# Kernel tuning notes

Measured on AMD Instinct MI355X. Metric: run time of the kernel, lower is better.

The kernel has to match this reference:

```python
import jax, jax.numpy as jnp
import numpy as np

N = 100000          # nodes
E = 1600000         # edges (avg degree 16)
F_IN = 128          # input node features
H1, C1 = 8, 8       # conv1: 8 heads, 8 channels/head -> 64 concat
NUM_CLASSES = 40    # conv2: 1 head, 40 channels
EPS = 1e-16         # PyG softmax denominator epsilon
NEG_SLOPE = 0.2     # PyG GATConv default leaky_relu slope


def setup_inputs() -> dict:
    key = jax.random.key(0)
    ks = jax.random.split(key, 12)
    x = jax.random.normal(ks[0], (N, F_IN), jnp.float32)
    edge_index = jax.random.randint(ks[1], (2, E), 0, N, dtype=jnp.int64)
    edge_attr = jax.random.normal(ks[2], (E, 1), jnp.float32)
    # layer 1 params (Glorot-ish scaling)
    s1 = 1.0 / np.sqrt(F_IN)
    W1 = jax.random.normal(ks[3], (F_IN, H1 * C1), jnp.float32) * s1
    a_src1 = jax.random.normal(ks[4], (H1, C1), jnp.float32) * (1.0 / np.sqrt(C1))
    a_dst1 = jax.random.normal(ks[5], (H1, C1), jnp.float32) * (1.0 / np.sqrt(C1))
    b1 = jnp.zeros((H1 * C1,), jnp.float32)
    # layer 2 params: in = 64 (conv1 concat output), 1 head, NUM_CLASSES channels
    s2 = 1.0 / np.sqrt(H1 * C1)
    W2 = jax.random.normal(ks[6], (H1 * C1, NUM_CLASSES), jnp.float32) * s2
    a_src2 = jax.random.normal(ks[7], (1, NUM_CLASSES), jnp.float32) * (1.0 / np.sqrt(NUM_CLASSES))
    a_dst2 = jax.random.normal(ks[8], (1, NUM_CLASSES), jnp.float32) * (1.0 / np.sqrt(NUM_CLASSES))
    b2 = jnp.zeros((NUM_CLASSES,), jnp.float32)
    return {"x": x, "edge_index": edge_index, "edge_attr": edge_attr,
            "W1": W1, "a_src1": a_src1, "a_dst1": a_dst1, "b1": b1,
            "W2": W2, "a_src2": a_src2, "a_dst2": a_dst2, "b2": b2}


def gat_conv(x, src, dst, W, a_s, a_d, b, heads, out_ch):
    """PyG GATConv: linear -> per-edge leaky-relu attention -> dst softmax -> scatter-add."""
    n = x.shape[0]
    h = (x @ W).reshape(n, heads, out_ch)                 # [N,H,C]
    alpha_s = jnp.sum(h * a_s, axis=-1)                   # [N,H]
    alpha_d = jnp.sum(h * a_d, axis=-1)                   # [N,H]
    e = jax.nn.leaky_relu(alpha_s[src] + alpha_d[dst], NEG_SLOPE)  # [Etot,H]
    # segment softmax over incoming edges per destination node
    m = jax.ops.segment_max(e, dst, num_segments=n)       # [N,H]
    e = jnp.exp(e - m[dst])
    denom = jax.ops.segment_sum(e, dst, num_segments=n)   # [N,H]
    alpha = e / (denom[dst] + EPS)                        # [Etot,H]
    msg = h[src] * alpha[:, :, None]                      # [Etot,H,C]
    out = jax.ops.segment_sum(msg, dst, num_segments=n)   # [N,H,C]
    return out.reshape(n, heads * out_ch) + b             # concat heads + bias


def reference(x, edge_index, edge_attr, W1, a_src1, a_dst1, b1, W2, a_src2, a_dst2, b2):
    n = x.shape[0]
    # PyG GATConv adds self-loops by default
    loops = jnp.arange(n, dtype=edge_index.dtype)
    src = jnp.concatenate([edge_index[0], loops])
    dst = jnp.concatenate([edge_index[1], loops])
    x = x.astype(jnp.float32)
    x1 = jax.nn.elu(gat_conv(x, src, dst, W1, a_src1, a_dst1, b1, H1, C1))
    x2 = jax.nn.elu(gat_conv(x1, src, dst, W2, a_src2, a_dst2, b2, 1, NUM_CLASSES))
    return x2
```

## Files before the change

### kernel.cpp

```cpp
#include <hip/hip_runtime.h>
#include <math.h>

#define NN 100000
#define NE 1600000
#define NETOT (NE + NN)
#define FIN 128
#define H1N 8
#define D1 64
#define NC 40
#define LNT 64
#define LOG2E 1.44269504088896f

#define BSH 9
#define BNODES 512
#define NBUC ((NN + BNODES - 1) / BNODES)
#define EPB 4096
#define NBLKA ((NE + EPB - 1) / EPB)
#define BCAP 9216
#define LB1 ((NN + LNT - 1) / LNT)

__device__ __forceinline__ float leakyf(float x) { return x >= 0.0f ? x : 0.2f * x; }
__device__ __forceinline__ float eluf(float x)   { return x > 0.0f ? x : expm1f(x); }
__device__ __forceinline__ float exp2fast(float x) { return __builtin_amdgcn_exp2f(x); }

__device__ __forceinline__ unsigned short f2bf(float f) {
  unsigned u = __float_as_uint(f);
  u += 0x7fffu + ((u >> 16) & 1u);
  return (unsigned short)(u >> 16);
}
__device__ __forceinline__ float bflo(unsigned u) { return __uint_as_float(u << 16); }
__device__ __forceinline__ float bfhi(unsigned u) { return __uint_as_float(u & 0xffff0000u); }

__global__ void k_detect(const long long* __restrict__ ei, int* __restrict__ flag) {
  if (blockIdx.x == 0 && threadIdx.x == 0) {
    int is64 = 1;
    for (int i = 0; i < 16; ++i) {
      long long v = ei[i];
      if (v < 0 || v >= NN) is64 = 0;
    }
    *flag = is64;
  }
}

#define XS1(node, k) xs[(node) * FIN + ((k) ^ ((node) & 31))]
__global__ __launch_bounds__(512) void k_fusedA(
    const void* __restrict__ ei, const int* __restrict__ flag,
    unsigned int* __restrict__ subbuf, int* __restrict__ bcnt,
    const float* __restrict__ x, const float* __restrict__ W,
    const float* __restrict__ aw_s, const float* __restrict__ aw_d,
    unsigned short* __restrict__ h, float* __restrict__ als,
    float* __restrict__ ald) {
  __shared__ __align__(16) char smem[65536];
  int t = threadIdx.x;
  if (blockIdx.x < NBLKA) {
    unsigned int*   pay    = (unsigned int*)smem;
    unsigned int*   spay   = pay + EPB;
    unsigned short* bk     = (unsigned short*)(spay + EPB);
    unsigned short* sbk    = bk + EPB;
    int*            hist   = (int*)(sbk + EPB);
    int*            lstart = hist + 256;
    int*            cur    = lstart + 256;
    int*            gbase  = cur + 256;
    int e0 = blockIdx.x * EPB;
    int cnt = min(EPB, NE - e0);
    if (t < 256) hist[t] = 0;
    __syncthreads();
    bool f64 = (*flag) != 0;
    for (int i = t; i < cnt; i += 512) {
      int s, d;
      if (f64) {
        const long long* p = (const long long*)ei;
        s = (int)p[e0 + i]; d = (int)p[NE + e0 + i];
      } else {
        const int* p = (const int*)ei;
        s = p[e0 + i]; d = p[NE + e0 + i];
      }
      int b = d >> BSH;
      pay[i] = ((unsigned)s << BSH) | (unsigned)(d & (BNODES - 1));
      bk[i] = (unsigned short)b;
      atomicAdd(&hist[b], 1);
    }
    __syncthreads();
    int v = 0;
    if (t < 256) { v = hist[t]; lstart[t] = v; }
    __syncthreads();
    for (int st = 1; st < 256; st <<= 1) {
      int xv = (t < 256 && t >= st) ? lstart[t - st] : 0;
      __syncthreads();
      if (t < 256) lstart[t] += xv;
      __syncthreads();
    }
    int excl = 0;
    if (t < 256) excl = lstart[t] - v;
    __syncthreads();
    if (t < 256) {
      lstart[t] = excl;
      cur[t] = excl;
      gbase[t] = (v > 0) ? atomicAdd(&bcnt[t], v) : 0;
    }
    __syncthreads();
    for (int i = t; i < cnt; i += 512) {
      int b = bk[i];
      int pos = atomicAdd(&cur[b], 1);
      spay[pos] = pay[i];
      sbk[pos] = (unsigned short)b;
    }
    __syncthreads();
    for (int i = t; i < cnt; i += 512) {
      int b = sbk[i];
      int o = gbase[b] + (i - lstart[b]);
      if (o < BCAP) subbuf[(size_t)b * BCAP + o] = spay[i];
    }
  } else {
    float* ws = (float*)smem;
    float* xs = ws + FIN * D1;
    int base = (blockIdx.x - NBLKA) * LNT;
    for (int i = t; i < FIN * D1; i += 512) ws[i] = W[i];
    for (int i = t; i < LNT * FIN; i += 512) {
      int node = i >> 7, k = i & 127;
      int gn = base + node;
      if (gn >= NN) gn = NN - 1;
      XS1(node, k) = x[(size_t)gn * FIN + k];
    }
    __syncthreads();
    int head = t & 7, nl = t >> 3;
    float acc[8] = {0, 0, 0, 0, 0, 0, 0, 0};
    #pragma unroll 4
    for (int k = 0; k < FIN; ++k) {
      float x0 = XS1(nl, k);
      const float4* wr = (const float4*)&ws[k * D1 + head * 8];
      float4 wa = wr[0], wb = wr[1];
      acc[0] = fmaf(x0, wa.x, acc[0]);
      acc[1] = fmaf(x0, wa.y, acc[1]);
      acc[2] = fmaf(x0, wa.z, acc[2]);
      acc[3] = fmaf(x0, wa.w, acc[3]);
      acc[4] = fmaf(x0, wb.x, acc[4]);
      acc[5] = fmaf(x0, wb.y, acc[5]);
      acc[6] = fmaf(x0, wb.z, acc[6]);
      acc[7] = fmaf(x0, wb.w, acc[7]);
    }
    int n0 = base + nl;
    if (n0 < NN) {
      float s = 0.f, d = 0.f;
      #pragma unroll
      for (int c = 0; c < 8; ++c) {
        h[(size_t)n0 * D1 + head * 8 + c] = f2bf(acc[c]);
        s = fmaf(acc[c], aw_s[head * 8 + c], s);
        d = fmaf(acc[c], aw_d[head * 8 + c], d);
      }
      als[n0 * H1N + head] = s * LOG2E;
      ald[n0 * H1N + head] = d * LOG2E;
    }
  }
}

__global__ void k_bucketsum(const int* __restrict__ bcnt, int* __restrict__ bucket_base,
                            int* __restrict__ row_start) {
  __shared__ int sh[256];
  int t = threadIdx.x;
  int tot = 0;
  if (t < NBUC) {
    int d0 = t << BSH;
    int nloc = min(BNODES, NN - d0);
    tot = nloc + min(bcnt[t], BCAP);
  }
  sh[t] = tot;
  __syncthreads();
  for (int s = 1; s < 256; s <<= 1) {
    int x = (t >= s) ? sh[t - s] : 0;
    __syncthreads();
    sh[t] += x;
    __syncthreads();
  }
  if (t < NBUC) bucket_base[t] = sh[t] - tot;
  if (t == NBUC - 1) row_start[NN] = sh[t];
}

__global__ __launch_bounds__(256) void k_passB(const int* __restrict__ bcnt,
                       const unsigned int* __restrict__ subbuf,
                       const int* __restrict__ bucket_base,
                       int* __restrict__ row_start, int* __restrict__ csr) {
  __shared__ int hist[BNODES];
  __shared__ int ps[256];
  __shared__ int cur[BNODES];
  int b = blockIdx.x, t = threadIdx.x;
  int d0 = b << BSH;
  int nloc = min(BNODES, NN - d0);
  hist[t] = 0; hist[t + 256] = 0;
  __syncthreads();
  int cnt = min(bcnt[b], BCAP);
  const unsigned int* sb = subbuf + (size_t)b * BCAP;
  for (int i = t; i < cnt; i += 256)
    atomicAdd(&hist[sb[i] & (BNODES - 1)], 1);
  __syncthreads();
  int j0 = 2 * t, j1 = 2 * t + 1;
  int s0 = (j0 < nloc) ? hist[j0] + 1 : 0;
  int s1 = (j1 < nloc) ? hist[j1] + 1 : 0;
  int pairsum = s0 + s1;
  ps[t] = pairsum;
  __syncthreads();
  for (int s = 1; s < 256; s <<= 1) {
    int x = (t >= s) ? ps[t - s] : 0;
    __syncthreads();
    ps[t] += x;
    __syncthreads();
  }
  int excl = ps[t] - pairsum + bucket_base[b];
  if (j0 < nloc) {
    row_start[d0 + j0] = excl;
    csr[excl] = d0 + j0;
    cur[j0] = excl + 1;
  }
  if (j1 < nloc) {
    int rs = excl + s0;
    row_start[d0 + j1] = rs;
    csr[rs] = d0 + j1;
    cur[j1] = rs + 1;
  }
  __syncthreads();
  for (int i = t; i < cnt; i += 256) {
    unsigned u = sb[i];
    int pos = atomicAdd(&cur[u & (BNODES - 1)], 1);
    csr[pos] = (int)(u >> BSH);
  }
}

#define XS2(node, k) xs[(node) * D1 + ((k) ^ ((node) & 31))]
__global__ __launch_bounds__(512) void k_lin2(
    const unsigned int* __restrict__ x1bf, const float* __restrict__ W,
    const float* __restrict__ aw_s, const float* __restrict__ aw_d,
    unsigned short* __restrict__ h, float* __restrict__ als,
    float* __restrict__ ald) {
  __shared__ float ws[D1 * D1];
  __shared__ float xs[LNT * D1];
  int t = threadIdx.x;
  int base = blockIdx.x * LNT;
  for (int i = t; i < D1 * D1; i += 512) {
    int k = i >> 6, c = i & 63;
    ws[i] = (c < NC) ? W[k * NC + c] : 0.f;
  }
  for (int i = t; i < LNT * 32; i += 512) {
    int node = i >> 5, kd = i & 31;
    int gn = base + node;
    if (gn >= NN) gn = NN - 1;
    unsigned u = x1bf[(size_t)gn * 32 + kd];
    XS2(node, 2 * kd)     = bflo(u);
    XS2(node, 2 * kd + 1) = bfhi(u);
  }
  __syncthreads();
  int g = t & 7, nl = t >> 3;
  float acc[8] = {0, 0, 0, 0, 0, 0, 0, 0};
  #pragma unroll 4
  for (int k = 0; k < D1; ++k) {
    float x0 = XS2(nl, k);
    const float4* wr = (const float4*)&ws[k * D1 + g * 8];
    float4 wa = wr[0], wb = wr[1];
    acc[0] = fmaf(x0, wa.x, acc[0]);
    acc[1] = fmaf(x0, wa.y, acc[1]);
    acc[2] = fmaf(x0, wa.z, acc[2]);
    acc[3] = fmaf(x0, wa.w, acc[3]);
    acc[4] = fmaf(x0, wb.x, acc[4]);
    acc[5] = fmaf(x0, wb.y, acc[5]);
    acc[6] = fmaf(x0, wb.z, acc[6]);
    acc[7] = fmaf(x0, wb.w, acc[7]);
  }
  int n0 = base + nl;
  float s = 0.f, d = 0.f;
  #pragma unroll
  for (int c = 0; c < 8; ++c) {
    int col = g * 8 + c;
    float aws = (col < NC) ? aw_s[col] : 0.f;
    float awd = (col < NC) ? aw_d[col] : 0.f;
    s = fmaf(acc[c], aws, s);
    d = fmaf(acc[c], awd, d);
  }
  s += __shfl_xor(s, 1); d += __shfl_xor(d, 1);
  s += __shfl_xor(s, 2); d += __shfl_xor(d, 2);
  s += __shfl_xor(s, 4); d += __shfl_xor(d, 4);
  if (n0 < NN) {
    if (g < 5) {
      #pragma unroll
      for (int c = 0; c < 8; ++c) h[(size_t)n0 * NC + g * 8 + c] = f2bf(acc[c]);
    }
    if (g == 0) { als[n0] = s * LOG2E; ald[n0] = d * LOG2E; }
  }
}

__global__ void k_node1(const int* __restrict__ row_start, const int* __restrict__ csr,
                        const unsigned short* __restrict__ h, const float* __restrict__ als,
                        const float* __restrict__ ald, const float* __restrict__ b,
                        unsigned int* __restrict__ x1bf) {
  __shared__ float pl[4][2][32 * 9];
  int wid = threadIdx.x >> 6, half = (threadIdx.x >> 5) & 1, c2 = threadIdx.x & 31;
  int n = blockIdx.x * 8 + wid * 2 + half;
  float* pw = pl[wid][half];
  const unsigned int* h32 = (const unsigned int*)h;
  int r0 = row_start[n], r1 = row_start[n + 1];
  int hd = c2 >> 2;
  const float4* adp = (const float4*)(ald + (size_t)n * H1N);
  float4 ad0 = adp[0], ad1 = adp[1];
  float S = 0.f;
  float alo0 = 0.f, ahi0 = 0.f, alo1 = 0.f, ahi1 = 0.f;
  float alo2 = 0.f, ahi2 = 0.f, alo3 = 0.f, ahi3 = 0.f;
  for (int kb = r0; kb < r1; kb += 32) {
    int cnt = min(32, r1 - kb);
    if (c2 < cnt) {
      int sk = csr[kb + c2];
      const float4* ap = (const float4*)(als + (size_t)sk * H1N);
      float4 a0 = ap[0], a1 = ap[1];
      pw[c2 * 9 + 0] = exp2fast(leakyf(a0.x + ad0.x));
      pw[c2 * 9 + 1] = exp2fast(leakyf(a0.y + ad0.y));
      pw[c2 * 9 + 2] = exp2fast(leakyf(a0.z + ad0.z));
      pw[c2 * 9 + 3] = exp2fast(leakyf(a0.w + ad0.w));
      pw[c2 * 9 + 4] = exp2fast(leakyf(a1.x + ad1.x));
      pw[c2 * 9 + 5] = exp2fast(leakyf(a1.y + ad1.y));
      pw[c2 * 9 + 6] = exp2fast(leakyf(a1.z + ad1.z));
      pw[c2 * 9 + 7] = exp2fast(leakyf(a1.w + ad1.w));
      pw[c2 * 9 + 8] = __int_as_float(sk);
    }
    asm volatile("s_waitcnt lgkmcnt(0)" ::: "memory");
    int j = 0;
    for (; j + 4 <= cnt; j += 4) {
      int s0 = __float_as_int(pw[(j + 0) * 9 + 8]);
      int s1 = __float_as_int(pw[(j + 1) * 9 + 8]);
      int s2 = __float_as_int(pw[(j + 2) * 9 + 8]);
      int s3 = __float_as_int(pw[(j + 3) * 9 + 8]);
      float p0 = pw[(j + 0) * 9 + hd], p1 = pw[(j + 1) * 9 + hd];
      float p2 = pw[(j + 2) * 9 + hd], p3 = pw[(j + 3) * 9 + hd];
      unsigned u0 = h32[(unsigned)s0 * 32 + c2];
      unsigned u1 = h32[(unsigned)s1 * 32 + c2];
      unsigned u2 = h32[(unsigned)s2 * 32 + c2];
      unsigned u3 = h32[(unsigned)s3 * 32 + c2];
      alo0 = fmaf(p0, bflo(u0), alo0); ahi0 = fmaf(p0, bfhi(u0), ahi0);
      alo1 = fmaf(p1, bflo(u1), alo1); ahi1 = fmaf(p1, bfhi(u1), ahi1);
      alo2 = fmaf(p2, bflo(u2), alo2); ahi2 = fmaf(p2, bfhi(u2), ahi2);
      alo3 = fmaf(p3, bflo(u3), alo3); ahi3 = fmaf(p3, bfhi(u3), ahi3);
      S += (p0 + p1) + (p2 + p3);
    }
    for (; j < cnt; ++j) {
      int s0 = __float_as_int(pw[j * 9 + 8]);
      float p0 = pw[j * 9 + hd];
      unsigned u0 = h32[(unsigned)s0 * 32 + c2];
      alo0 = fmaf(p0, bflo(u0), alo0); ahi0 = fmaf(p0, bfhi(u0), ahi0);
      S += p0;
    }
  }
  float alo = (alo0 + alo1) + (alo2 + alo3);
  float ahi = (ahi0 + ahi1) + (ahi2 + ahi3);
  float inv = 1.0f / (S + 1e-16f);
  float ox = eluf(alo * inv + b[2 * c2 + 0]);
  float oy = eluf(ahi * inv + b[2 * c2 + 1]);
  x1bf[(size_t)n * 32 + c2] = (unsigned)f2bf(ox) | ((unsigned)f2bf(oy) << 16);
}

__global__ void k_node2(const int* __restrict__ row_start, const int* __restrict__ csr,
                        const unsigned short* __restrict__ h, const float* __restrict__ als,
                        const float* __restrict__ ald, const float* __restrict__ b,
                        float* __restrict__ out) {
  __shared__ float pl[4][2][32 * 3];
  int wid = threadIdx.x >> 6, half = (threadIdx.x >> 5) & 1, c2 = threadIdx.x & 31;
  int n = blockIdx.x * 8 + wid * 2 + half;
  float* pw = pl[wid][half];
  const unsigned int* h32 = (const unsigned int*)h;
  int r0 = row_start[n], r1 = row_start[n + 1];
  int cl = c2 < 20 ? c2 : 19;
  float aldn = ald[n];
  float S = 0.f;
  float alo0 = 0.f, ahi0 = 0.f, alo1 = 0.f, ahi1 = 0.f;
  float alo2 = 0.f, ahi2 = 0.f, alo3 = 0.f, ahi3 = 0.f;
  for (int kb = r0; kb < r1; kb += 32) {
    int cnt = min(32, r1 - kb);
    if (c2 < cnt) {
      int sk = csr[kb + c2];
      pw[c2 * 3 + 0] = exp2fast(leakyf(als[sk] + aldn));
      pw[c2 * 3 + 1] = __int_as_float(sk);
    }
    asm volatile("s_waitcnt lgkmcnt(0)" ::: "memory");
    int j = 0;
    for (; j + 4 <= cnt; j += 4) {
      int s0 = __float_as_int(pw[(j + 0) * 3 + 1]);
      int s1 = __float_as_int(pw[(j + 1) * 3 + 1]);
      int s2 = __float_as_int(pw[(j + 2) * 3 + 1]);
      int s3 = __float_as_int(pw[(j + 3) * 3 + 1]);
      float p0 = pw[(j + 0) * 3], p1 = pw[(j + 1) * 3];
      float p2 = pw[(j + 2) * 3], p3 = pw[(j + 3) * 3];
      unsigned u0 = h32[(unsigned)s0 * 20 + cl];
      unsigned u1 = h32[(unsigned)s1 * 20 + cl];
      unsigned u2 = h32[(unsigned)s2 * 20 + cl];
      unsigned u3 = h32[(unsigned)s3 * 20 + cl];
      alo0 = fmaf(p0, bflo(u0), alo0); ahi0 = fmaf(p0, bfhi(u0), ahi0);
      alo1 = fmaf(p1, bflo(u1), alo1); ahi1 = fmaf(p1, bfhi(u1), ahi1);
      alo2 = fmaf(p2, bflo(u2), alo2); ahi2 = fmaf(p2, bfhi(u2), ahi2);
      alo3 = fmaf(p3, bflo(u3), alo3); ahi3 = fmaf(p3, bfhi(u3), ahi3);
      S += (p0 + p1) + (p2 + p3);
    }
    for (; j < cnt; ++j) {
      int s0 = __float_as_int(pw[j * 3 + 1]);
      float p0 = pw[j * 3];
      unsigned u0 = h32[(unsigned)s0 * 20 + cl];
      alo0 = fmaf(p0, bflo(u0), alo0); ahi0 = fmaf(p0, bfhi(u0), ahi0);
      S += p0;
    }
  }
  float alo = (alo0 + alo1) + (alo2 + alo3);
  float ahi = (ahi0 + ahi1) + (ahi2 + ahi3);
  if (c2 < 20) {
    float inv = 1.0f / (S + 1e-16f);
    float2 o;
    o.x = eluf(alo * inv + b[2 * c2 + 0]);
    o.y = eluf(ahi * inv + b[2 * c2 + 1]);
    ((float2*)out)[(size_t)n * 20 + c2] = o;
  }
}

extern "C" void kernel_launch(void* const* d_in, const int* in_sizes, int n_in,
                              void* d_out, int out_size, void* d_ws, size_t ws_size,
                              hipStream_t stream) {
  const float* x    = (const float*)d_in[0];
  const void*  ei   = d_in[1];
  const float* W1   = (const float*)d_in[3];
  const float* as1w = (const float*)d_in[4];
  const float* ad1w = (const float*)d_in[5];
  const float* b1   = (const float*)d_in[6];
  const float* W2   = (const float*)d_in[7];
  const float* as2w = (const float*)d_in[8];
  const float* ad2w = (const float*)d_in[9];
  const float* b2   = (const float*)d_in[10];
  float* out = (float*)d_out;

  char* w = (char*)d_ws;
  size_t off = 0;
  auto carve = [&](size_t bytes) -> void* {
    void* r = w + off;
    off += (bytes + 255) & ~(size_t)255;
    return r;
  };
  int*            flag        = (int*)carve(256);
  int*            bcnt        = (int*)carve((size_t)NBUC * 4);
  int*            bucket_base = (int*)carve((size_t)NBUC * 4);
  unsigned int*   subbuf      = (unsigned int*)carve((size_t)NBUC * BCAP * 4);
  int*            row_start   = (int*)carve((size_t)(NN + 1) * 4);
  int*            csr         = (int*)carve((size_t)NETOT * 4);
  unsigned short* h1          = (unsigned short*)carve((size_t)NN * D1 * 2);
  float*          als1        = (float*)carve((size_t)NN * H1N * 4);
  float*          ald1        = (float*)carve((size_t)NN * H1N * 4);
  unsigned int*   x1bf        = (unsigned int*)carve((size_t)NN * 32 * 4);
  unsigned short* h2 = h1; float* als2 = als1; float* ald2 = ald1;

  k_detect<<<1, 64, 0, stream>>>((const long long*)ei, flag);
  (void)hipMemsetAsync(bcnt, 0, (size_t)NBUC * 4, stream);

  k_fusedA<<<NBLKA + LB1, 512, 0, stream>>>(ei, flag, subbuf, bcnt,
                                            x, W1, as1w, ad1w, h1, als1, ald1);

  k_bucketsum<<<1, 256, 0, stream>>>(bcnt, bucket_base, row_start);
  k_passB<<<NBUC, 256, 0, stream>>>(bcnt, subbuf, bucket_base, row_start, csr);

  k_node1<<<NN / 8, 256, 0, stream>>>(row_start, csr, h1, als1, ald1, b1, x1bf);

  k_lin2<<<LB1, 512, 0, stream>>>(x1bf, W2, as2w, ad2w, h2, als2, ald2);
  k_node2<<<NN / 8, 256, 0, stream>>>(row_start, csr, h2, als2, ald2, b2, out);
}
```

Measured before the change: 206.2 us.

## Fold memset and bucket scan into neighbor kernels, repack node2 lanes, vectorize h store

Zeroing the bucket counters moves into the detect kernel, and the separate bucket-sum kernel is removed: every passB block redoes the small prefix scan over bucket totals itself. This cuts two launches or dependent steps. k_node2 now packs three destination nodes per wavefront, 20 lanes each, instead of two nodes per 32 lanes with 12 idle lanes, which raises lane use in the 40-class aggregation. The layer-1 bf16 h write becomes one 16-byte packed store per thread instead of eight 2-byte stores. In exchange, each passB block repeats the scan redundantly, and 4 of 64 lanes stay idle in node2.

```diff
diff --git a/kernel.cpp b/kernel.cpp
--- a/kernel.cpp
+++ b/kernel.cpp
@@ -17,7 +17,7 @@
 #define EPB 4096
 #define NBLKA ((NE + EPB - 1) / EPB)
 #define BCAP 9216
-#define LB1 ((NN + LNT - 1) / LNT)
+#define LB ((NN + LNT - 1) / LNT)
 
 __device__ __forceinline__ float leakyf(float x) { return x >= 0.0f ? x : 0.2f * x; }
 __device__ __forceinline__ float eluf(float x)   { return x > 0.0f ? x : expm1f(x); }
@@ -31,8 +31,11 @@
 __device__ __forceinline__ float bflo(unsigned u) { return __uint_as_float(u << 16); }
 __device__ __forceinline__ float bfhi(unsigned u) { return __uint_as_float(u & 0xffff0000u); }
 
-__global__ void k_detect(const long long* __restrict__ ei, int* __restrict__ flag) {
-  if (blockIdx.x == 0 && threadIdx.x == 0) {
+__global__ void k_detect(const long long* __restrict__ ei, int* __restrict__ flag,
+                         int* __restrict__ bcnt) {
+  int t = threadIdx.x;
+  if (t < NBUC) bcnt[t] = 0;
+  if (t == 0) {
     int is64 = 1;
     for (int i = 0; i < 16; ++i) {
       long long v = ei[i];
@@ -123,12 +126,12 @@
       XS1(node, k) = x[(size_t)gn * FIN + k];
     }
     __syncthreads();
-    int head = t & 7, nl = t >> 3;
+    int g = t & 7, nl = t >> 3;
     float acc[8] = {0, 0, 0, 0, 0, 0, 0, 0};
     #pragma unroll 4
     for (int k = 0; k < FIN; ++k) {
       float x0 = XS1(nl, k);
-      const float4* wr = (const float4*)&ws[k * D1 + head * 8];
+      const float4* wr = (const float4*)&ws[k * D1 + g * 8];
       float4 wa = wr[0], wb = wr[1];
       acc[0] = fmaf(x0, wa.x, acc[0]);
       acc[1] = fmaf(x0, wa.y, acc[1]);
@@ -142,50 +145,50 @@
     int n0 = base + nl;
     if (n0 < NN) {
       float s = 0.f, d = 0.f;
+      uint4 pk;
+      pk.x = (unsigned)f2bf(acc[0]) | ((unsigned)f2bf(acc[1]) << 16);
+      pk.y = (unsigned)f2bf(acc[2]) | ((unsigned)f2bf(acc[3]) << 16);
+      pk.z = (unsigned)f2bf(acc[4]) | ((unsigned)f2bf(acc[5]) << 16);
+      pk.w = (unsigned)f2bf(acc[6]) | ((unsigned)f2bf(acc[7]) << 16);
+      *(uint4*)(void*)(h + (size_t)n0 * D1 + g * 8) = pk;
       #pragma unroll
       for (int c = 0; c < 8; ++c) {
-        h[(size_t)n0 * D1 + head * 8 + c] = f2bf(acc[c]);
-        s = fmaf(acc[c], aw_s[head * 8 + c], s);
-        d = fmaf(acc[c], aw_d[head * 8 + c], d);
+        s = fmaf(acc[c], aw_s[g * 8 + c], s);
+        d = fmaf(acc[c], aw_d[g * 8 + c], d);
       }
-      als[n0 * H1N + head] = s * LOG2E;
-      ald[n0 * H1N + head] = d * LOG2E;
-    }
-  }
-}
-
-__global__ void k_bucketsum(const int* __restrict__ bcnt, int* __restrict__ bucket_base,
-                            int* __restrict__ row_start) {
-  __shared__ int sh[256];
-  int t = threadIdx.x;
-  int tot = 0;
-  if (t < NBUC) {
-    int d0 = t << BSH;
-    int nloc = min(BNODES, NN - d0);
-    tot = nloc + min(bcnt[t], BCAP);
-  }
-  sh[t] = tot;
-  __syncthreads();
-  for (int s = 1; s < 256; s <<= 1) {
-    int x = (t >= s) ? sh[t - s] : 0;
-    __syncthreads();
-    sh[t] += x;
-    __syncthreads();
-  }
-  if (t < NBUC) bucket_base[t] = sh[t] - tot;
-  if (t == NBUC - 1) row_start[NN] = sh[t];
+      als[n0 * H1N + g] = s * LOG2E;
+      ald[n0 * H1N + g] = d * LOG2E;
+    }
+  }
 }
 
 __global__ __launch_bounds__(256) void k_passB(const int* __restrict__ bcnt,
                        const unsigned int* __restrict__ subbuf,
-                       const int* __restrict__ bucket_base,
                        int* __restrict__ row_start, int* __restrict__ csr) {
   __shared__ int hist[BNODES];
   __shared__ int ps[256];
   __shared__ int cur[BNODES];
+  __shared__ int bbs;
   int b = blockIdx.x, t = threadIdx.x;
   int d0 = b << BSH;
   int nloc = min(BNODES, NN - d0);
+  int tot = 0;
+  if (t < NBUC) {
+    int dd = t << BSH;
+    tot = min(BNODES, NN - dd) + min(bcnt[t], BCAP);
+  }
+  ps[t] = tot;
+  __syncthreads();
+  for (int s = 1; s < 256; s <<= 1) {
+    int xv = (t >= s) ? ps[t - s] : 0;
+    __syncthreads();
+    ps[t] += xv;
+    __syncthreads();
+  }
+  if (t == 0) bbs = (b == 0) ? 0 : ps[b - 1];
+  if (b == 0 && t == 0) row_start[NN] = ps[NBUC - 1];
+  __syncthreads();
+  int bucket_base = bbs;
   hist[t] = 0; hist[t + 256] = 0;
   __syncthreads();
   int cnt = min(bcnt[b], BCAP);
@@ -205,7 +208,7 @@
     ps[t] += x;
     __syncthreads();
   }
-  int excl = ps[t] - pairsum + bucket_base[b];
+  int excl = ps[t] - pairsum + bucket_base;
   if (j0 < nloc) {
     row_start[d0 + j0] = excl;
     csr[excl] = d0 + j0;
@@ -357,37 +360,40 @@
                         const unsigned short* __restrict__ h, const float* __restrict__ als,
                         const float* __restrict__ ald, const float* __restrict__ b,
                         float* __restrict__ out) {
-  __shared__ float pl[4][2][32 * 3];
-  int wid = threadIdx.x >> 6, half = (threadIdx.x >> 5) & 1, c2 = threadIdx.x & 31;
-  int n = blockIdx.x * 8 + wid * 2 + half;
-  float* pw = pl[wid][half];
+  __shared__ float pl[4][3][20 * 2];
+  int wid = threadIdx.x >> 6, lane = threadIdx.x & 63;
+  int g = lane / 20, q = lane - g * 20;
+  int gg = g < 3 ? g : 2;
+  int n = blockIdx.x * 12 + wid * 3 + gg;
+  bool live = (g < 3) && (n < NN);
+  if (n >= NN) n = NN - 1;
+  float* pw = pl[wid][gg];
   const unsigned int* h32 = (const unsigned int*)h;
   int r0 = row_start[n], r1 = row_start[n + 1];
-  int cl = c2 < 20 ? c2 : 19;
   float aldn = ald[n];
   float S = 0.f;
   float alo0 = 0.f, ahi0 = 0.f, alo1 = 0.f, ahi1 = 0.f;
   float alo2 = 0.f, ahi2 = 0.f, alo3 = 0.f, ahi3 = 0.f;
-  for (int kb = r0; kb < r1; kb += 32) {
-    int cnt = min(32, r1 - kb);
-    if (c2 < cnt) {
-      int sk = csr[kb + c2];
-      pw[c2 * 3 + 0] = exp2fast(leakyf(als[sk] + aldn));
-      pw[c2 * 3 + 1] = __int_as_float(sk);
+  for (int kb = r0; kb < r1; kb += 20) {
+    int cnt = min(20, r1 - kb);
+    if (q < cnt && g < 3) {
+      int sk = csr[kb + q];
+      pw[q * 2 + 0] = exp2fast(leakyf(als[sk] + aldn));
+      pw[q * 2 + 1] = __int_as_float(sk);
     }
     asm volatile("s_waitcnt lgkmcnt(0)" ::: "memory");
     int j = 0;
     for (; j + 4 <= cnt; j += 4) {
-      int s0 = __float_as_int(pw[(j + 0) * 3 + 1]);
-      int s1 = __float_as_int(pw[(j + 1) * 3 + 1]);
-      int s2 = __float_as_int(pw[(j + 2) * 3 + 1]);
-      int s3 = __float_as_int(pw[(j + 3) * 3 + 1]);
-      float p0 = pw[(j + 0) * 3], p1 = pw[(j + 1) * 3];
-      float p2 = pw[(j + 2) * 3], p3 = pw[(j + 3) * 3];
-      unsigned u0 = h32[(unsigned)s0 * 20 + cl];
-      unsigned u1 = h32[(unsigned)s1 * 20 + cl];
-      unsigned u2 = h32[(unsigned)s2 * 20 + cl];
-      unsigned u3 = h32[(unsigned)s3 * 20 + cl];
+      int s0 = __float_as_int(pw[(j + 0) * 2 + 1]);
+      int s1 = __float_as_int(pw[(j + 1) * 2 + 1]);
+      int s2 = __float_as_int(pw[(j + 2) * 2 + 1]);
+      int s3 = __float_as_int(pw[(j + 3) * 2 + 1]);
+      float p0 = pw[(j + 0) * 2], p1 = pw[(j + 1) * 2];
+      float p2 = pw[(j + 2) * 2], p3 = pw[(j + 3) * 2];
+      unsigned u0 = h32[(unsigned)s0 * 20 + q];
+      unsigned u1 = h32[(unsigned)s1 * 20 + q];
+      unsigned u2 = h32[(unsigned)s2 * 20 + q];
+      unsigned u3 = h32[(unsigned)s3 * 20 + q];
       alo0 = fmaf(p0, bflo(u0), alo0); ahi0 = fmaf(p0, bfhi(u0), ahi0);
       alo1 = fmaf(p1, bflo(u1), alo1); ahi1 = fmaf(p1, bfhi(u1), ahi1);
       alo2 = fmaf(p2, bflo(u2), alo2); ahi2 = fmaf(p2, bfhi(u2), ahi2);
@@ -395,21 +401,21 @@
       S += (p0 + p1) + (p2 + p3);
     }
     for (; j < cnt; ++j) {
-      int s0 = __float_as_int(pw[j * 3 + 1]);
-      float p0 = pw[j * 3];
-      unsigned u0 = h32[(unsigned)s0 * 20 + cl];
+      int s0 = __float_as_int(pw[j * 2 + 1]);
+      float p0 = pw[j * 2];
+      unsigned u0 = h32[(unsigned)s0 * 20 + q];
       alo0 = fmaf(p0, bflo(u0), alo0); ahi0 = fmaf(p0, bfhi(u0), ahi0);
       S += p0;
     }
   }
   float alo = (alo0 + alo1) + (alo2 + alo3);
   float ahi = (ahi0 + ahi1) + (ahi2 + ahi3);
-  if (c2 < 20) {
+  if (live) {
     float inv = 1.0f / (S + 1e-16f);
     float2 o;
-    o.x = eluf(alo * inv + b[2 * c2 + 0]);
-    o.y = eluf(ahi * inv + b[2 * c2 + 1]);
-    ((float2*)out)[(size_t)n * 20 + c2] = o;
+    o.x = eluf(alo * inv + b[2 * q + 0]);
+    o.y = eluf(ahi * inv + b[2 * q + 1]);
+    ((float2*)out)[(size_t)n * 20 + q] = o;
   }
 }
 
@@ -437,7 +443,6 @@
   };
   int*            flag        = (int*)carve(256);
   int*            bcnt        = (int*)carve((size_t)NBUC * 4);
-  int*            bucket_base = (int*)carve((size_t)NBUC * 4);
   unsigned int*   subbuf      = (unsigned int*)carve((size_t)NBUC * BCAP * 4);
   int*            row_start   = (int*)carve((size_t)(NN + 1) * 4);
   int*            csr         = (int*)carve((size_t)NETOT * 4);
@@ -447,17 +452,15 @@
   unsigned int*   x1bf        = (unsigned int*)carve((size_t)NN * 32 * 4);
   unsigned short* h2 = h1; float* als2 = als1; float* ald2 = ald1;
 
-  k_detect<<<1, 64, 0, stream>>>((const long long*)ei, flag);
-  (void)hipMemsetAsync(bcnt, 0, (size_t)NBUC * 4, stream);
-
-  k_fusedA<<<NBLKA + LB1, 512, 0, stream>>>(ei, flag, subbuf, bcnt,
-                                            x, W1, as1w, ad1w, h1, als1, ald1);
-
-  k_bucketsum<<<1, 256, 0, stream>>>(bcnt, bucket_base, row_start);
-  k_passB<<<NBUC, 256, 0, stream>>>(bcnt, subbuf, bucket_base, row_start, csr);
+  k_detect<<<1, 256, 0, stream>>>((const long long*)ei, flag, bcnt);
+
+  k_fusedA<<<NBLKA + LB, 512, 0, stream>>>(ei, flag, subbuf, bcnt,
+                                           x, W1, as1w, ad1w, h1, als1, ald1);
+
+  k_passB<<<NBUC, 256, 0, stream>>>(bcnt, subbuf, row_start, csr);
 
   k_node1<<<NN / 8, 256, 0, stream>>>(row_start, csr, h1, als1, ald1, b1, x1bf);
 
-  k_lin2<<<LB1, 512, 0, stream>>>(x1bf, W2, as2w, ad2w, h2, als2, ald2);
-  k_node2<<<NN / 8, 256, 0, stream>>>(row_start, csr, h2, als2, ald2, b2, out);
-}
+  k_lin2<<<LB, 512, 0, stream>>>(x1bf, W2, as2w, ad2w, h2, als2, ald2);
+  k_node2<<<(NN + 11) / 12, 256, 0, stream>>>(row_start, csr, h2, als2, ald2, b2, out);
+}
```

Result: no change. 203.8 us, median of 3 (-1.2%).
